# Optimization experiments

Measured on AMD Instinct MI355X. Metric: run time of the kernel, lower is better.

## Reference

```python
import jax, jax.numpy as jnp
import numpy as np

B, T, C = 4, 2048, 1024
N_HEAD = 16
HEAD_DIM = C // N_HEAD


def setup_inputs() -> dict:
    key = jax.random.key(0)
    k1, k2, k3 = jax.random.split(key, 3)
    x = jax.random.normal(k1, (B, T, C), dtype=jnp.float32)
    w_attn = jax.random.normal(k2, (C, 3 * C), dtype=jnp.float32) * 0.02
    b_attn = jnp.zeros((3 * C,), dtype=jnp.float32)
    # c_proj init stddev = 0.02 / sqrt(2 * n_layer), n_layer = 24
    w_proj = jax.random.normal(k3, (C, C), dtype=jnp.float32) * (0.02 / np.sqrt(48.0))
    b_proj = jnp.zeros((C,), dtype=jnp.float32)
    return {"x": x, "w_attn": w_attn, "b_attn": b_attn,
            "w_proj": w_proj, "b_proj": b_proj}


def reference(x, w_attn, b_attn, w_proj, b_proj):
    Bx, Tx, Cx = x.shape
    scale = 1.0 / jnp.sqrt(jnp.asarray(HEAD_DIM, dtype=x.dtype))
    qkv = x @ w_attn + b_attn                      # [B,T,3C]
    qkv = qkv.reshape(Bx, Tx, 3, N_HEAD, HEAD_DIM)
    q, k, v = qkv[:, :, 0], qkv[:, :, 1], qkv[:, :, 2]  # each [B,T,H,D]
    att = jnp.einsum('bthd,bThd->bhtT', q, k) * scale   # [B,H,T,T]
    mask = jnp.tril(jnp.ones((Tx, Tx), dtype=x.dtype)).reshape(1, 1, Tx, Tx)
    att = att * mask - 1e10 * (1 - mask)
    att = jax.nn.softmax(att, axis=-1)
    y = jnp.einsum('bhtT,bThd->bthd', att, v)      # [B,T,H,D]
    y = y.reshape(Bx, Tx, Cx)
    return y @ w_proj + b_proj
```

## Files before the change

### kernel.cpp

```cpp
#include <hip/hip_runtime.h>
#include <hip/hip_bf16.h>


typedef __attribute__((ext_vector_type(8)))  __bf16 bf16x8;
typedef __attribute__((ext_vector_type(2)))  float  f32x2;
typedef __attribute__((ext_vector_type(4)))  float  f32x4;
typedef __attribute__((ext_vector_type(16))) float  f32x16;
typedef __attribute__((ext_vector_type(4)))  unsigned int u32x4;

#define AS1C(p) ((const __attribute__((address_space(1))) unsigned int*)(p))
#define AS3(p)  ((__attribute__((address_space(3))) unsigned int*)(p))

__device__ __forceinline__ unsigned short f2bfu(float f){
  __hip_bfloat16 h = __float2bfloat16(f);
  return __builtin_bit_cast(unsigned short, h);
}

__device__ __forceinline__ void plswapu(unsigned int &a, unsigned int &b){
  asm("v_permlane32_swap_b32 %0, %1" : "+v"(a), "+v"(b));
}
__device__ __forceinline__ unsigned int cvtpk(float lo, float hi){
  unsigned int r;
  asm("v_cvt_pk_bf16_f32 %0, %1, %2" : "=v"(r) : "v"(lo), "v"(hi));
  return r;
}
__device__ __forceinline__ float max3f(float a, float b, float c){
  float r;
  asm("v_max3_f32 %0, %1, %2, %3" : "=v"(r) : "v"(a), "v"(b), "v"(c));
  return r;
}


__global__ __launch_bounds__(256)
void prep_all(const float* __restrict__ x, __hip_bfloat16* __restrict__ xb,
              const float* __restrict__ w_attn, __hip_bfloat16* __restrict__ wattnT,
              const float* __restrict__ w_proj, __hip_bfloat16* __restrict__ wprojT)
{
  __shared__ float tile[32][33];
  const int idx = blockIdx.x;
  if (idx < 2048){
    const int n4 = 8388608/4;
    for (int i = idx*256 + threadIdx.x; i < n4; i += 2048*256){
      float4 v = reinterpret_cast<const float4*>(x)[i];
      ushort4 u;
      u.x = f2bfu(v.x); u.y = f2bfu(v.y); u.z = f2bfu(v.z); u.w = f2bfu(v.w);
      reinterpret_cast<ushort4*>(xb)[i] = u;
    }
  } else {
    const float* in; __hip_bfloat16* out; int C, R, bx, by;
    if (idx < 5120){
      const int f = idx - 2048;
      in = w_attn; out = wattnT; R = 1024; C = 3072;
      bx = f % 96; by = f / 96;
    } else {
      const int f = idx - 5120;
      in = w_proj; out = wprojT; R = 1024; C = 1024;
      bx = f & 31; by = f >> 5;
    }
    const int tx = threadIdx.x & 31, ty = threadIdx.x >> 5;
    const int c0 = bx*32, r0 = by*32;
    for (int i = ty; i < 32; i += 8)
      tile[i][tx] = in[(size_t)(r0+i)*C + c0 + tx];
    __syncthreads();
    for (int i = ty; i < 32; i += 8)
      out[(size_t)(c0+i)*R + r0 + tx] = __float2bfloat16(tile[tx][i]);
  }
}


#define QSCALE 0.1803368801111244f

__device__ __forceinline__ void stage_ab(const __hip_bfloat16* __restrict__ A,
                                         const __hip_bfloat16* __restrict__ Bt,
                                         int m0, int n0, int K, int kt,
                                         __hip_bfloat16* sA, __hip_bfloat16* sB,
                                         int w, int l)
{
  const int k0 = kt*32;
  #pragma unroll
  for (int qq = 0; qq < 2; ++qq){
    const int c = qq*256 + w*64 + l;
    const int row = c>>2, kc = c&3;
    const int kcs = kc ^ ((row>>1)&3);
    __builtin_amdgcn_global_load_lds(AS1C(A  + (size_t)(m0+row)*K + k0 + 8*kcs),
                                     AS3(sA + (qq*256 + w*64)*8), 16, 0, 0);
    __builtin_amdgcn_global_load_lds(AS1C(Bt + (size_t)(n0+row)*K + k0 + 8*kcs),
                                     AS3(sB + (qq*256 + w*64)*8), 16, 0, 0);
  }
}

template<int EPI>
__global__ __launch_bounds__(256)
void gemm_bf16(const __hip_bfloat16* __restrict__ A,
               const __hip_bfloat16* __restrict__ Bt,
               const float* __restrict__ bias,
               int M, int N, int K,
               __hip_bfloat16* __restrict__ q_s,
               __hip_bfloat16* __restrict__ k_s,
               __hip_bfloat16* __restrict__ vT_s,
               float* __restrict__ outf)
{
  __shared__ __align__(16) __hip_bfloat16 sA[2][128*32];
  __shared__ __align__(16) __hip_bfloat16 sB[2][128*32];
  const int tid = threadIdx.x, w = tid>>6, l = tid&63, g = l>>4, li = l&15;
  const int wm = w>>1, wn = w&1;
  const int sw = (li>>1)&3;

  const int nwg = gridDim.x, cpx = nwg >> 3;
  const int swz = (blockIdx.x & 7)*cpx + (blockIdx.x >> 3);
  const int nbx = N >> 7;
  const int GM = 4, chunk = GM * nbx;
  const int grp = swz / chunk, pos = swz - grp*chunk;
  const int m0 = (grp*GM + (pos & (GM-1)))*128;
  const int n0 = (pos >> 2)*128;

  f32x4 acc[4][4] = {};

  const int NT = K >> 5;
  stage_ab(A, Bt, m0, n0, K, 0, sA[0], sB[0], w, l);
  int cur = 0;

  for (int kt = 0; kt < NT; ++kt){
    __syncthreads();
    if (kt + 1 < NT)
      stage_ab(A, Bt, m0, n0, K, kt+1, sA[cur^1], sB[cur^1], w, l);

    bf16x8 af[4], bfr[4];
    #pragma unroll
    for (int mi = 0; mi < 4; ++mi)
      af[mi] = *reinterpret_cast<const bf16x8*>(sA[cur] + (wm*64 + mi*16 + li)*32 + 8*(g ^ sw));
    #pragma unroll
    for (int ni = 0; ni < 4; ++ni)
      bfr[ni] = *reinterpret_cast<const bf16x8*>(sB[cur] + (wn*64 + ni*16 + li)*32 + 8*(g ^ sw));
    #pragma unroll
    for (int mi = 0; mi < 4; ++mi)
      #pragma unroll
      for (int ni = 0; ni < 4; ++ni)
        acc[mi][ni] = __builtin_amdgcn_mfma_f32_16x16x32_bf16(af[mi], bfr[ni], acc[mi][ni], 0, 0, 0);
    cur ^= 1;
  }

  #pragma unroll
  for (int ni = 0; ni < 4; ++ni){
    const int col = n0 + wn*64 + ni*16 + li;
    const float bv = bias[col];
    #pragma unroll
    for (int mi = 0; mi < 4; ++mi){
      #pragma unroll
      for (int e = 0; e < 4; ++e){
        const int row = m0 + wm*64 + mi*16 + 4*g + e;
        const float val = acc[mi][ni][e] + bv;
        if (EPI == 0){
          const int three = col >> 10, h = (col >> 6) & 15, d = col & 63;
          const int b = row >> 11, t = row & 2047;
          const int bh = b*16 + h;
          if (three == 0)      q_s[((size_t)bh*2048 + t)*64 + d]  = __float2bfloat16(val*QSCALE);
          else if (three == 1) k_s[((size_t)bh*2048 + t)*64 + d]  = __float2bfloat16(val);
          else                 vT_s[((size_t)bh*64 + d)*2048 + t] = __float2bfloat16(val);
        } else {
          outf[(size_t)row*N + col] = val;
        }
      }
    }
  }
}


__device__ __forceinline__ void stage_kv64(const __hip_bfloat16* __restrict__ k_s,
                                           const __hip_bfloat16* __restrict__ vT_s,
                                           size_t base, int j,
                                           __hip_bfloat16* sk, __hip_bfloat16* svt,
                                           int tid)
{
  #pragma unroll
  for (int it = 0; it < 4; ++it){
    const int c = it*128 + tid;
    const int r = c>>3, cc = c&7;
    __builtin_amdgcn_global_load_lds(AS1C(k_s  + base + (size_t)(j*64 + r)*64 + 8*(cc ^ (r&7))),
                                     AS3(sk  + c*8), 16, 0, 0);
    __builtin_amdgcn_global_load_lds(AS1C(vT_s + base + (size_t)r*2048 + j*64 + 8*(cc ^ (r&7))),
                                     AS3(svt + c*8), 16, 0, 0);
  }
}

__device__ __forceinline__ bf16x8 ldtile(const __hip_bfloat16* t, int row, int chunk){
  return *reinterpret_cast<const bf16x8*>(t + row*64 + ((chunk ^ (row&7))*8));
}

__global__ __launch_bounds__(128, 2)
void flash_attn(const __hip_bfloat16* __restrict__ q_s,
                const __hip_bfloat16* __restrict__ k_s,
                const __hip_bfloat16* __restrict__ vT_s,
                __hip_bfloat16* __restrict__ y_s)
{
  __shared__ __align__(16) __hip_bfloat16 sk [2][64*64];
  __shared__ __align__(16) __hip_bfloat16 svt[3][64*64];

  const int tid = threadIdx.x, w = tid>>6, l = tid&63;
  const int lq = l&31, hf = l>>5, h4 = 4*hf;
  const int bid = blockIdx.x;
  const int xcd = bid & 7, sl = (bid>>3) & 7;
  const int v = 31 - (bid >> 6);
  const int bh = xcd*8 + sl;
  const size_t base = (size_t)bh * (2048*64);
  const int b = bh >> 4, hh = bh & 15;

  const int tw = 2*v + w;
  const int jd = v;
  const int qabs = 32*tw + lq;
  const int rel = 32*w + lq;

  bf16x8 qf[4];
  #pragma unroll
  for (int ks = 0; ks < 4; ++ks)
    qf[ks] = *reinterpret_cast<const bf16x8*>(q_s + base + (size_t)qabs*64 + 16*ks + 8*hf);

  f32x16 o0 = {}, o1 = {};
  float mrun = -1e30f, lrun = 0.f;
  bf16x8 pfrA[4], pfrB[4];

  __hip_bfloat16 *skC = sk[0],  *skN = sk[1];
  __hip_bfloat16 *svP = svt[2], *svC = svt[0], *svN = svt[1];

  stage_kv64(k_s, vT_s, base, 0, skC, svC, tid);

  #define ATTN_STEP(J, PFR_P, PFR_C)                                          \
  {                                                                           \
    const int j_ = (J);                                                       \
    __syncthreads();                                                          \
    if (j_ + 1 <= jd)                                                         \
      stage_kv64(k_s, vT_s, base, j_+1, skN, svN, tid);                       \
    f32x16 s0 = {}, s1 = {};                                                  \
    __builtin_amdgcn_s_setprio(1);                                            \
    _Pragma("unroll")                                                         \
    for (int ks = 0; ks < 4; ++ks){                                           \
      bf16x8 kf0 = ldtile(skC, lq,      2*ks + hf);                           \
      s0 = __builtin_amdgcn_mfma_f32_32x32x16_bf16(kf0, qf[ks], s0, 0,0,0);   \
      bf16x8 kf1 = ldtile(skC, 32 + lq, 2*ks + hf);                           \
      s1 = __builtin_amdgcn_mfma_f32_32x32x16_bf16(kf1, qf[ks], s1, 0,0,0);   \
    }                                                                         \
    if (j_ > 0){                                                              \
      _Pragma("unroll")                                                       \
      for (int ks = 0; ks < 4; ++ks){                                         \
        bf16x8 vf0 = ldtile(svP, lq,      2*ks + hf);                         \
        o0 = __builtin_amdgcn_mfma_f32_32x32x16_bf16(vf0, PFR_C[ks], o0,0,0,0);\
        bf16x8 vf1 = ldtile(svP, 32 + lq, 2*ks + hf);                         \
        o1 = __builtin_amdgcn_mfma_f32_32x32x16_bf16(vf1, PFR_C[ks], o1,0,0,0);\
      }                                                                       \
    }                                                                         \
    __builtin_amdgcn_s_setprio(0);                                            \
                       \
    f32x2 pf2[16];                                                            \
    _Pragma("unroll")                                                         \
    for (int i = 0; i < 8; ++i){                                              \
      pf2[i]     = (f32x2){ s0[2*i], s0[2*i+1] };                             \
      pf2[8 + i] = (f32x2){ s1[2*i], s1[2*i+1] };                             \
    }                                                                         \
    if (j_ == jd){                                                            \
      _Pragma("unroll")                                                       \
      for (int i = 0; i < 16; ++i){                                           \
        const int a = i >> 3;                                                 \
        const int r0i = (i & 7)*2, r1i = r0i + 1;                             \
        const int kv0 = 32*a + (r0i&3) + 8*(r0i>>2) + h4;                     \
        const int kv1 = 32*a + (r1i&3) + 8*(r1i>>2) + h4;                     \
        pf2[i].x = (kv0 <= rel) ? pf2[i].x : -1e30f;                          \
        pf2[i].y = (kv1 <= rel) ? pf2[i].y : -1e30f;                          \
      }                                                                       \
    }                                                                         \
    float t0 = max3f(PFX(0),PFX(1),PFX(2)),   t1 = max3f(PFX(3),PFX(4),PFX(5));   \
    float t2 = max3f(PFX(6),PFX(7),PFX(8)),   t3 = max3f(PFX(9),PFX(10),PFX(11)); \
    float t4 = max3f(PFX(12),PFX(13),PFX(14)),t5 = max3f(PFX(15),PFX(16),PFX(17));\
    float t6 = max3f(PFX(18),PFX(19),PFX(20)),t7 = max3f(PFX(21),PFX(22),PFX(23));\
    float t8 = max3f(PFX(24),PFX(25),PFX(26)),t9 = max3f(PFX(27),PFX(28),PFX(29));\
    float t10 = fmaxf(PFX(30),PFX(31));                                       \
    float u0 = max3f(t0,t1,t2), u1 = max3f(t3,t4,t5), u2 = max3f(t6,t7,t8);   \
    float u3 = fmaxf(t9,t10);                                                 \
    float pm = fmaxf(max3f(u0,u1,u2), u3);                                    \
    if (!__all(pm - mrun <= 8.0f)){                                           \
      pm = fmaxf(pm, __shfl_xor(pm, 32));                                     \
      const float nm = fmaxf(mrun, pm);                                       \
      const float corr = exp2f(mrun - nm);                                    \
      mrun = nm;                                                              \
      o0 *= corr; o1 *= corr;                                                 \
      lrun *= corr;                                                           \
    }                                                                         \
    const f32x2 negm = { -mrun, -mrun };                                      \
    _Pragma("unroll")                                                         \
    for (int i = 0; i < 16; ++i) pf2[i] = pf2[i] + negm;                      \
    _Pragma("unroll")                                                         \
    for (int i = 0; i < 16; ++i){                                             \
      pf2[i].x = exp2f(pf2[i].x);                                             \
      pf2[i].y = exp2f(pf2[i].y);                                             \
    }                                                                         \
    f32x2 q8[8];                                                              \
    _Pragma("unroll")                                                         \
    for (int i = 0; i < 8; ++i) q8[i] = pf2[i] + pf2[8+i];                    \
    f32x2 q4a = q8[0]+q8[4], q4b = q8[1]+q8[5], q4c = q8[2]+q8[6], q4d = q8[3]+q8[7];\
    f32x2 q2a = q4a+q4c, q2b = q4b+q4d;                                       \
    f32x2 q1 = q2a+q2b;                                                       \
    float psum = q1.x + q1.y;                                                 \
    psum += __shfl_xor(psum, 32);                                             \
    lrun += psum;                                                             \
    unsigned int wds[16];                                                     \
    _Pragma("unroll")                                                         \
    for (int k = 0; k < 16; ++k) wds[k] = cvtpk(pf2[k].x, pf2[k].y);          \
    _Pragma("unroll")                                                         \
    for (int a = 0; a < 2; ++a)                                               \
      _Pragma("unroll")                                                       \
      for (int bl = 0; bl < 2; ++bl){                                         \
        plswapu(wds[a*8 + 4*bl    ], wds[a*8 + 4*bl + 2]);                    \
        plswapu(wds[a*8 + 4*bl + 1], wds[a*8 + 4*bl + 3]);                    \
      }                                                                       \
    _Pragma("unroll")                                                         \
    for (int B = 0; B < 4; ++B){                                              \
      u32x4 tt = { wds[4*B], wds[4*B+1], wds[4*B+2], wds[4*B+3] };            \
      PFR_P[B] = __builtin_bit_cast(bf16x8, tt);                              \
    }                                                                         \
                 \
    { __hip_bfloat16* t_ = skC; skC = skN; skN = t_; }                        \
    { __hip_bfloat16* t_ = svP; svP = svC; svC = svN; svN = t_; }             \
  }

  #define PFX(K) (((K)&1) ? pf2[(K)>>1].y : pf2[(K)>>1].x)
  int j = 0;
  #pragma unroll 1
  for (; j + 1 <= jd; j += 2){
    ATTN_STEP(j,   pfrA, pfrB);
    ATTN_STEP(j+1, pfrB, pfrA);
  }
  if (j <= jd)
    ATTN_STEP(j, pfrA, pfrB);
  #undef PFX
  #undef ATTN_STEP

  if ((jd & 1) == 0){
    #pragma unroll
    for (int ks = 0; ks < 4; ++ks){
      bf16x8 vf0 = ldtile(svP, lq,      2*ks + hf);
      o0 = __builtin_amdgcn_mfma_f32_32x32x16_bf16(vf0, pfrA[ks], o0, 0, 0, 0);
      bf16x8 vf1 = ldtile(svP, 32 + lq, 2*ks + hf);
      o1 = __builtin_amdgcn_mfma_f32_32x32x16_bf16(vf1, pfrA[ks], o1, 0, 0, 0);
    }
  } else {
    #pragma unroll
    for (int ks = 0; ks < 4; ++ks){
      bf16x8 vf0 = ldtile(svP, lq,      2*ks + hf);
      o0 = __builtin_amdgcn_mfma_f32_32x32x16_bf16(vf0, pfrB[ks], o0, 0, 0, 0);
      bf16x8 vf1 = ldtile(svP, 32 + lq, 2*ks + hf);
      o1 = __builtin_amdgcn_mfma_f32_32x32x16_bf16(vf1, pfrB[ks], o1, 0, 0, 0);
    }
  }

  const float inv = 1.f / lrun;
  __hip_bfloat16* yp = y_s + ((size_t)(b*2048 + qabs))*1024 + hh*64;
  #pragma unroll
  for (int i = 0; i < 8; ++i){
    const int d = (2*i & 3) + 8*(i>>1) + h4;
    *reinterpret_cast<unsigned int*>(yp + d)      = cvtpk(o0[2*i]*inv, o0[2*i+1]*inv);
    *reinterpret_cast<unsigned int*>(yp + 32 + d) = cvtpk(o1[2*i]*inv, o1[2*i+1]*inv);
  }
}


extern "C" void kernel_launch(void* const* d_in, const int* in_sizes, int n_in,
                              void* d_out, int out_size, void* d_ws, size_t ws_size,
                              hipStream_t stream)
{
  const float* x      = (const float*)d_in[0];
  const float* w_attn = (const float*)d_in[1];
  const float* b_attn = (const float*)d_in[2];
  const float* w_proj = (const float*)d_in[3];
  const float* b_proj = (const float*)d_in[4];
  float* out = (float*)d_out;
  char* ws = (char*)d_ws;

  __hip_bfloat16* xb     = (__hip_bfloat16*)(ws + 0);
  __hip_bfloat16* wattnT = (__hip_bfloat16*)(ws + 16777216);
  __hip_bfloat16* wprojT = (__hip_bfloat16*)(ws + 23068672);
  __hip_bfloat16* q_s    = (__hip_bfloat16*)(ws + 25165824);
  __hip_bfloat16* k_s    = (__hip_bfloat16*)(ws + 41943040);
  __hip_bfloat16* vT_s   = (__hip_bfloat16*)(ws + 58720256);
  __hip_bfloat16* y_s    = xb;

  prep_all<<<6144, 256, 0, stream>>>(x, xb, w_attn, wattnT, w_proj, wprojT);

  gemm_bf16<0><<<1536, 256, 0, stream>>>(
      xb, wattnT, b_attn, 8192, 3072, 1024, q_s, k_s, vT_s, (float*)nullptr);

  flash_attn<<<2048, 128, 0, stream>>>(q_s, k_s, vT_s, y_s);

  gemm_bf16<1><<<512, 256, 0, stream>>>(
      y_s, wprojT, b_proj, 8192, 1024, 1024,
      (__hip_bfloat16*)nullptr, (__hip_bfloat16*)nullptr, (__hip_bfloat16*)nullptr, out);
}
```

Before: 186.7 us.

## Share each staged K/V tile across four waves covering 128 query rows

The flash-attention block grows from 2 to 4 waves, so each block covers 128 query rows. Every staged 64-row K/V tile is now reused by twice as many waves, which halves global-to-LDS traffic per query. The grid is halved and the q-block launch order is remapped to balance the causal workload across blocks. In exchange, the two lower waves sit idle on the last diagonal step, with per-wave guards on the QK and PV work. Launch bounds change to 256 threads with 3 blocks, which may add register pressure.

```diff
diff --git a/kernel.cpp b/kernel.cpp
--- a/kernel.cpp
+++ b/kernel.cpp
@@ -173,8 +173,8 @@
                                            int tid)
 {
   #pragma unroll
-  for (int it = 0; it < 4; ++it){
-    const int c = it*128 + tid;
+  for (int it = 0; it < 2; ++it){
+    const int c = it*256 + tid;
     const int r = c>>3, cc = c&7;
     __builtin_amdgcn_global_load_lds(AS1C(k_s  + base + (size_t)(j*64 + r)*64 + 8*(cc ^ (r&7))),
                                      AS3(sk  + c*8), 16, 0, 0);
@@ -187,7 +187,7 @@
   return *reinterpret_cast<const bf16x8*>(t + row*64 + ((chunk ^ (row&7))*8));
 }
 
-__global__ __launch_bounds__(128, 2)
+__global__ __launch_bounds__(256, 3)
 void flash_attn(const __hip_bfloat16* __restrict__ q_s,
                 const __hip_bfloat16* __restrict__ k_s,
                 const __hip_bfloat16* __restrict__ vT_s,
@@ -200,15 +200,17 @@
   const int lq = l&31, hf = l>>5, h4 = 4*hf;
   const int bid = blockIdx.x;
   const int xcd = bid & 7, sl = (bid>>3) & 7;
-  const int v = 31 - (bid >> 6);
+  const int q = bid >> 6;
+  const int v = (q < 4 || q >= 12) ? (15 - q) : ((q < 8) ? q + 4 : q - 4);
   const int bh = xcd*8 + sl;
   const size_t base = (size_t)bh * (2048*64);
   const int b = bh >> 4, hh = bh & 15;
 
-  const int tw = 2*v + w;
-  const int jd = v;
+  const int tw = 4*v + w;
+  const int jd = 2*v + (w >> 1);
+  const int jmax = 2*v + 1;
   const int qabs = 32*tw + lq;
-  const int rel = 32*w + lq;
+  const int rel = 32*(w & 1) + lq;
 
   bf16x8 qf[4];
   #pragma unroll
@@ -228,18 +230,20 @@
   {                                                                           \
     const int j_ = (J);                                                       \
     __syncthreads();                                                          \
-    if (j_ + 1 <= jd)                                                         \
+    if (j_ + 1 <= jmax)                                                       \
       stage_kv64(k_s, vT_s, base, j_+1, skN, svN, tid);                       \
     f32x16 s0 = {}, s1 = {};                                                  \
     __builtin_amdgcn_s_setprio(1);                                            \
-    _Pragma("unroll")                                                         \
-    for (int ks = 0; ks < 4; ++ks){                                           \
-      bf16x8 kf0 = ldtile(skC, lq,      2*ks + hf);                           \
-      s0 = __builtin_amdgcn_mfma_f32_32x32x16_bf16(kf0, qf[ks], s0, 0,0,0);   \
-      bf16x8 kf1 = ldtile(skC, 32 + lq, 2*ks + hf);                           \
-      s1 = __builtin_amdgcn_mfma_f32_32x32x16_bf16(kf1, qf[ks], s1, 0,0,0);   \
+    if (j_ <= jd){                                                            \
+      _Pragma("unroll")                                                       \
+      for (int ks = 0; ks < 4; ++ks){                                         \
+        bf16x8 kf0 = ldtile(skC, lq,      2*ks + hf);                         \
+        s0 = __builtin_amdgcn_mfma_f32_32x32x16_bf16(kf0, qf[ks], s0, 0,0,0); \
+        bf16x8 kf1 = ldtile(skC, 32 + lq, 2*ks + hf);                         \
+        s1 = __builtin_amdgcn_mfma_f32_32x32x16_bf16(kf1, qf[ks], s1, 0,0,0); \
+      }                                                                       \
     }                                                                         \
-    if (j_ > 0){                                                              \
+    if (j_ > 0 && j_ - 1 <= jd){                                              \
       _Pragma("unroll")                                                       \
       for (int ks = 0; ks < 4; ++ks){                                         \
         bf16x8 vf0 = ldtile(svP, lq,      2*ks + hf);                         \
@@ -249,72 +253,73 @@
       }                                                                       \
     }                                                                         \
     __builtin_amdgcn_s_setprio(0);                                            \
-                       \
-    f32x2 pf2[16];                                                            \
-    _Pragma("unroll")                                                         \
-    for (int i = 0; i < 8; ++i){                                              \
-      pf2[i]     = (f32x2){ s0[2*i], s0[2*i+1] };                             \
-      pf2[8 + i] = (f32x2){ s1[2*i], s1[2*i+1] };                             \
-    }                                                                         \
-    if (j_ == jd){                                                            \
+    if (j_ <= jd){                                                            \
+      f32x2 pf2[16];                                                          \
+      _Pragma("unroll")                                                       \
+      for (int i = 0; i < 8; ++i){                                            \
+        pf2[i]     = (f32x2){ s0[2*i], s0[2*i+1] };                           \
+        pf2[8 + i] = (f32x2){ s1[2*i], s1[2*i+1] };                           \
+      }                                                                       \
+      if (j_ == jd){                                                          \
+        _Pragma("unroll")                                                     \
+        for (int i = 0; i < 16; ++i){                                         \
+          const int a = i >> 3;                                               \
+          const int r0i = (i & 7)*2, r1i = r0i + 1;                           \
+          const int kv0 = 32*a + (r0i&3) + 8*(r0i>>2) + h4;                   \
+          const int kv1 = 32*a + (r1i&3) + 8*(r1i>>2) + h4;                   \
+          pf2[i].x = (kv0 <= rel) ? pf2[i].x : -1e30f;                        \
+          pf2[i].y = (kv1 <= rel) ? pf2[i].y : -1e30f;                        \
+        }                                                                     \
+      }                                                                       \
+      float t0 = max3f(PFX(0),PFX(1),PFX(2)),   t1 = max3f(PFX(3),PFX(4),PFX(5));   \
+      float t2 = max3f(PFX(6),PFX(7),PFX(8)),   t3 = max3f(PFX(9),PFX(10),PFX(11)); \
+      float t4 = max3f(PFX(12),PFX(13),PFX(14)),t5 = max3f(PFX(15),PFX(16),PFX(17));\
+      float t6 = max3f(PFX(18),PFX(19),PFX(20)),t7 = max3f(PFX(21),PFX(22),PFX(23));\
+      float t8 = max3f(PFX(24),PFX(25),PFX(26)),t9 = max3f(PFX(27),PFX(28),PFX(29));\
+      float t10 = fmaxf(PFX(30),PFX(31));                                     \
+      float u0 = max3f(t0,t1,t2), u1 = max3f(t3,t4,t5), u2 = max3f(t6,t7,t8); \
+      float u3 = fmaxf(t9,t10);                                               \
+      float pm = fmaxf(max3f(u0,u1,u2), u3);                                  \
+      if (!__all(pm - mrun <= 8.0f)){                                         \
+        pm = fmaxf(pm, __shfl_xor(pm, 32));                                   \
+        const float nm = fmaxf(mrun, pm);                                     \
+        const float corr = exp2f(mrun - nm);                                  \
+        mrun = nm;                                                            \
+        o0 *= corr; o1 *= corr;                                               \
+        lrun *= corr;                                                         \
+      }                                                                       \
+      const f32x2 negm = { -mrun, -mrun };                                    \
+      _Pragma("unroll")                                                       \
+      for (int i = 0; i < 16; ++i) pf2[i] = pf2[i] + negm;                    \
       _Pragma("unroll")                                                       \
       for (int i = 0; i < 16; ++i){                                           \
-        const int a = i >> 3;                                                 \
-        const int r0i = (i & 7)*2, r1i = r0i + 1;                             \
-        const int kv0 = 32*a + (r0i&3) + 8*(r0i>>2) + h4;                     \
-        const int kv1 = 32*a + (r1i&3) + 8*(r1i>>2) + h4;                     \
-        pf2[i].x = (kv0 <= rel) ? pf2[i].x : -1e30f;                          \
-        pf2[i].y = (kv1 <= rel) ? pf2[i].y : -1e30f;                          \
-      }                                                                       \
-    }                                                                         \
-    float t0 = max3f(PFX(0),PFX(1),PFX(2)),   t1 = max3f(PFX(3),PFX(4),PFX(5));   \
-    float t2 = max3f(PFX(6),PFX(7),PFX(8)),   t3 = max3f(PFX(9),PFX(10),PFX(11)); \
-    float t4 = max3f(PFX(12),PFX(13),PFX(14)),t5 = max3f(PFX(15),PFX(16),PFX(17));\
-    float t6 = max3f(PFX(18),PFX(19),PFX(20)),t7 = max3f(PFX(21),PFX(22),PFX(23));\
-    float t8 = max3f(PFX(24),PFX(25),PFX(26)),t9 = max3f(PFX(27),PFX(28),PFX(29));\
-    float t10 = fmaxf(PFX(30),PFX(31));                                       \
-    float u0 = max3f(t0,t1,t2), u1 = max3f(t3,t4,t5), u2 = max3f(t6,t7,t8);   \
-    float u3 = fmaxf(t9,t10);                                                 \
-    float pm = fmaxf(max3f(u0,u1,u2), u3);                                    \
-    if (!__all(pm - mrun <= 8.0f)){                                           \
-      pm = fmaxf(pm, __shfl_xor(pm, 32));                                     \
-      const float nm = fmaxf(mrun, pm);                                       \
-      const float corr = exp2f(mrun - nm);                                    \
-      mrun = nm;                                                              \
-      o0 *= corr; o1 *= corr;                                                 \
-      lrun *= corr;                                                           \
-    }                                                                         \
-    const f32x2 negm = { -mrun, -mrun };                                      \
-    _Pragma("unroll")                                                         \
-    for (int i = 0; i < 16; ++i) pf2[i] = pf2[i] + negm;                      \
-    _Pragma("unroll")                                                         \
-    for (int i = 0; i < 16; ++i){                                             \
-      pf2[i].x = exp2f(pf2[i].x);                                             \
-      pf2[i].y = exp2f(pf2[i].y);                                             \
-    }                                                                         \
-    f32x2 q8[8];                                                              \
-    _Pragma("unroll")                                                         \
-    for (int i = 0; i < 8; ++i) q8[i] = pf2[i] + pf2[8+i];                    \
-    f32x2 q4a = q8[0]+q8[4], q4b = q8[1]+q8[5], q4c = q8[2]+q8[6], q4d = q8[3]+q8[7];\
-    f32x2 q2a = q4a+q4c, q2b = q4b+q4d;                                       \
-    f32x2 q1 = q2a+q2b;                                                       \
-    float psum = q1.x + q1.y;                                                 \
-    psum += __shfl_xor(psum, 32);                                             \
-    lrun += psum;                                                             \
-    unsigned int wds[16];                                                     \
-    _Pragma("unroll")                                                         \
-    for (int k = 0; k < 16; ++k) wds[k] = cvtpk(pf2[k].x, pf2[k].y);          \
-    _Pragma("unroll")                                                         \
-    for (int a = 0; a < 2; ++a)                                               \
-      _Pragma("unroll")                                                       \
-      for (int bl = 0; bl < 2; ++bl){                                         \
-        plswapu(wds[a*8 + 4*bl    ], wds[a*8 + 4*bl + 2]);                    \
-        plswapu(wds[a*8 + 4*bl + 1], wds[a*8 + 4*bl + 3]);                    \
-      }                                                                       \
-    _Pragma("unroll")                                                         \
-    for (int B = 0; B < 4; ++B){                                              \
-      u32x4 tt = { wds[4*B], wds[4*B+1], wds[4*B+2], wds[4*B+3] };            \
-      PFR_P[B] = __builtin_bit_cast(bf16x8, tt);                              \
+        pf2[i].x = exp2f(pf2[i].x);                                           \
+        pf2[i].y = exp2f(pf2[i].y);                                           \
+      }                                                                       \
+      f32x2 q8[8];                                                            \
+      _Pragma("unroll")                                                       \
+      for (int i = 0; i < 8; ++i) q8[i] = pf2[i] + pf2[8+i];                  \
+      f32x2 q4a = q8[0]+q8[4], q4b = q8[1]+q8[5], q4c = q8[2]+q8[6], q4d = q8[3]+q8[7];\
+      f32x2 q2a = q4a+q4c, q2b = q4b+q4d;                                     \
+      f32x2 q1 = q2a+q2b;                                                     \
+      float psum = q1.x + q1.y;                                               \
+      psum += __shfl_xor(psum, 32);                                           \
+      lrun += psum;                                                           \
+      unsigned int wds[16];                                                   \
+      _Pragma("unroll")                                                       \
+      for (int k = 0; k < 16; ++k) wds[k] = cvtpk(pf2[k].x, pf2[k].y);        \
+      _Pragma("unroll")                                                       \
+      for (int a = 0; a < 2; ++a)                                             \
+        _Pragma("unroll")                                                     \
+        for (int bl = 0; bl < 2; ++bl){                                       \
+          plswapu(wds[a*8 + 4*bl    ], wds[a*8 + 4*bl + 2]);                  \
+          plswapu(wds[a*8 + 4*bl + 1], wds[a*8 + 4*bl + 3]);                  \
+        }                                                                     \
+      _Pragma("unroll")                                                       \
+      for (int B = 0; B < 4; ++B){                                            \
+        u32x4 tt = { wds[4*B], wds[4*B+1], wds[4*B+2], wds[4*B+3] };          \
+        PFR_P[B] = __builtin_bit_cast(bf16x8, tt);                            \
+      }                                                                       \
     }                                                                         \
                  \
     { __hip_bfloat16* t_ = skC; skC = skN; skN = t_; }                        \
@@ -322,26 +327,15 @@
   }
 
   #define PFX(K) (((K)&1) ? pf2[(K)>>1].y : pf2[(K)>>1].x)
-  int j = 0;
   #pragma unroll 1
-  for (; j + 1 <= jd; j += 2){
+  for (int j = 0; j + 1 <= jmax; j += 2){
     ATTN_STEP(j,   pfrA, pfrB);
     ATTN_STEP(j+1, pfrB, pfrA);
   }
-  if (j <= jd)
-    ATTN_STEP(j, pfrA, pfrB);
   #undef PFX
   #undef ATTN_STEP
 
-  if ((jd & 1) == 0){
-    #pragma unroll
-    for (int ks = 0; ks < 4; ++ks){
-      bf16x8 vf0 = ldtile(svP, lq,      2*ks + hf);
-      o0 = __builtin_amdgcn_mfma_f32_32x32x16_bf16(vf0, pfrA[ks], o0, 0, 0, 0);
-      bf16x8 vf1 = ldtile(svP, 32 + lq, 2*ks + hf);
-      o1 = __builtin_amdgcn_mfma_f32_32x32x16_bf16(vf1, pfrA[ks], o1, 0, 0, 0);
-    }
-  } else {
+  if (jd == jmax){
     #pragma unroll
     for (int ks = 0; ks < 4; ++ks){
       bf16x8 vf0 = ldtile(svP, lq,      2*ks + hf);
@@ -387,7 +381,7 @@
   gemm_bf16<0><<<1536, 256, 0, stream>>>(
       xb, wattnT, b_attn, 8192, 3072, 1024, q_s, k_s, vT_s, (float*)nullptr);
 
-  flash_attn<<<2048, 128, 0, stream>>>(q_s, k_s, vT_s, y_s);
+  flash_attn<<<1024, 256, 0, stream>>>(q_s, k_s, vT_s, y_s);
 
   gemm_bf16<1><<<512, 256, 0, stream>>>(
       y_s, wprojT, b_proj, 8192, 1024, 1024,
```

Measured after the change: 209.1 us. 12.0% more time.
